# Kernel tuning notes

Hardware: AMD Instinct MI355X
Metric: run time of the kernel (lower is better)

The kernel has to match this reference:

```python
import jax, jax.numpy as jnp
import numpy as np

L = 4          # n_layers
D_MODEL = 512
D_STATE = 32
D_INNER = 1024  # expand=2
D_CONV = 4
DT_RANK = 32    # ceil(d_model/16)
B = 8
T = 512


def setup_inputs() -> dict:
    key = jax.random.key(0)
    ks = jax.random.split(key, 12)
    s = 0.02
    x = jax.random.normal(ks[0], (B, T, D_MODEL), jnp.float32)
    in_w = jax.random.normal(ks[1], (L, D_MODEL, 2 * D_INNER), jnp.float32) * s
    conv_w = jax.random.normal(ks[2], (L, D_INNER, D_CONV), jnp.float32) * s
    conv_b = jnp.zeros((L, D_INNER), jnp.float32)
    xproj_w = jax.random.normal(ks[3], (L, D_INNER, DT_RANK + 2 * D_STATE), jnp.float32) * s
    dt_w = jax.random.normal(ks[4], (L, DT_RANK, D_INNER), jnp.float32) * s
    dt_b = jax.random.normal(ks[5], (L, D_INNER), jnp.float32) * 0.1
    # S4D-real init: A_log = log(1..d_state) per channel
    A_log = jnp.log(jnp.broadcast_to(jnp.arange(1, D_STATE + 1, dtype=jnp.float32), (L, D_INNER, D_STATE)))
    Dp = jnp.ones((L, D_INNER), jnp.float32)
    layer_out_w = jax.random.normal(ks[6], (L, D_INNER, D_MODEL), jnp.float32) * s
    ln_w = jnp.ones((L, D_MODEL), jnp.float32)
    ln_b = jnp.zeros((L, D_MODEL), jnp.float32)
    proj_w = jax.random.normal(ks[7], (D_MODEL, D_MODEL), jnp.float32) * s
    proj_b = jnp.zeros((D_MODEL,), jnp.float32)
    return dict(x=x, in_w=in_w, conv_w=conv_w, conv_b=conv_b, xproj_w=xproj_w,
                dt_w=dt_w, dt_b=dt_b, A_log=A_log, Dp=Dp, layer_out_w=layer_out_w,
                ln_w=ln_w, ln_b=ln_b, proj_w=proj_w, proj_b=proj_b)


def _layernorm(x, w, b, eps=1e-5):
    mu = jnp.mean(x, axis=-1, keepdims=True)
    var = jnp.mean(jnp.square(x - mu), axis=-1, keepdims=True)
    return (x - mu) * jax.lax.rsqrt(var + eps) * w + b


def _selective_scan(u, delta, A, Bm, Cm, D):
    # u, delta: (B,T,di); A: (di,ds); Bm, Cm: (B,T,ds); D: (di,)
    def step(h, inp):
        d_t, B_t, C_t, u_t = inp                      # (B,di),(B,ds),(B,ds),(B,di)
        dA = jnp.exp(d_t[..., None] * A)               # (B,di,ds)
        h = dA * h + (d_t * u_t)[..., None] * B_t[:, None, :]
        y = jnp.einsum('bdn,bn->bd', h, C_t)
        return h, y
    h0 = jnp.zeros((u.shape[0], A.shape[0], A.shape[1]), u.dtype)
    xs = (jnp.swapaxes(delta, 0, 1), jnp.swapaxes(Bm, 0, 1),
          jnp.swapaxes(Cm, 0, 1), jnp.swapaxes(u, 0, 1))
    _, ys = jax.lax.scan(step, h0, xs)                 # ys: (T,B,di)
    return jnp.swapaxes(ys, 0, 1) + u * D


def _mamba_layer(x, in_w, conv_w, conv_b, xproj_w, dt_w, dt_b, A_log, D, out_w):
    xz = x @ in_w                                      # (B,T,2*di)
    u, z = jnp.split(xz, 2, axis=-1)
    # causal depthwise conv1d over time
    uc = jnp.swapaxes(u, 1, 2)                         # (B,di,T)
    uc = jnp.pad(uc, ((0, 0), (0, 0), (D_CONV - 1, 0)))
    uc = jax.lax.conv_general_dilated(
        uc, conv_w[:, None, :], (1,), 'VALID',
        feature_group_count=D_INNER,
        dimension_numbers=('NCH', 'OIH', 'NCH')) + conv_b[None, :, None]
    u = jax.nn.silu(jnp.swapaxes(uc, 1, 2))            # (B,T,di)
    x_dbl = u @ xproj_w                                # (B,T,dt_rank+2*ds)
    dt, Bm, Cm = jnp.split(x_dbl, [DT_RANK, DT_RANK + D_STATE], axis=-1)
    delta = jax.nn.softplus(dt @ dt_w + dt_b)          # (B,T,di)
    A = -jnp.exp(A_log)                                # (di,ds)
    y = _selective_scan(u, delta, A, Bm, Cm, D)
    y = y * jax.nn.silu(z)
    return y @ out_w                                   # (B,T,d_model)


def reference(x, in_w, conv_w, conv_b, xproj_w, dt_w, dt_b, A_log, Dp,
              layer_out_w, ln_w, ln_b, proj_w, proj_b):
    for i in range(L):
        h = _layernorm(x, ln_w[i], ln_b[i])
        x = _mamba_layer(h, in_w[i], conv_w[i], conv_b[i], xproj_w[i],
                         dt_w[i], dt_b[i], A_log[i], Dp[i], layer_out_w[i]) + x
    return x @ proj_w + proj_b
```

## Files before the change

### kernel.cpp

```cpp
#include <hip/hip_runtime.h>
#include <math.h>

#define LNUM 4
#define DM 512
#define DS 32
#define DI 1024
#define DTR 32
#define NB 8
#define NT 512
#define MROWS (NB*NT)
#define NCH (NB*DI)
#define NCK 32
#define TCH (NT/NCK)
#define SSTR 257
#define L2E 1.44269504f

typedef __attribute__((ext_vector_type(8))) short short8;
typedef __attribute__((ext_vector_type(4))) float floatx4;
typedef unsigned short ushort_t;

__device__ __forceinline__ float sigmoidf_(float x){ return 1.f/(1.f+__expf(-x)); }
__device__ __forceinline__ float exp2f_(float x){ return __builtin_amdgcn_exp2f(x); }
__device__ __forceinline__ float bf2f(ushort_t u){ return __uint_as_float(((unsigned)u)<<16); }

__device__ __forceinline__ unsigned short rne_bf16(float f){
  unsigned int u = __float_as_uint(f);
  u += 0x7fffu + ((u >> 16) & 1u);
  return (unsigned short)(u >> 16);
}

__device__ __forceinline__ void load_lds16(const void* g, void* l){
  __builtin_amdgcn_global_load_lds(
      (const __attribute__((address_space(1))) void*)g,
      (__attribute__((address_space(3))) void*)l, 16, 0, 0);
}

__global__ __launch_bounds__(256) void lnz_k(const float* __restrict__ x,
    const float* __restrict__ w, const float* __restrict__ b,
    ushort_t* __restrict__ out, float* __restrict__ xdbl)
{
  int bid = blockIdx.x;
  if (bid >= MROWS){
    int g = (bid - MROWS)*256 + threadIdx.x;
    ((floatx4*)xdbl)[g] = (floatx4){0.f,0.f,0.f,0.f};
    return;
  }
  const float* xr = x + (size_t)bid*DM;
  float v0 = xr[threadIdx.x];
  float v1 = xr[threadIdx.x + 256];
  float s = v0+v1, sq = v0*v0+v1*v1;
  #pragma unroll
  for (int off=32; off>0; off>>=1) { s += __shfl_xor(s, off, 64); sq += __shfl_xor(sq, off, 64); }
  __shared__ float ls[4], lq[4];
  int wid = threadIdx.x >> 6;
  if ((threadIdx.x & 63)==0){ ls[wid]=s; lq[wid]=sq; }
  __syncthreads();
  s  = ls[0]+ls[1]+ls[2]+ls[3];
  sq = lq[0]+lq[1]+lq[2]+lq[3];
  float mean = s * (1.f/DM);
  float var  = sq * (1.f/DM) - mean*mean;
  float rstd = rsqrtf(var + 1e-5f);
  int c0 = threadIdx.x, c1 = threadIdx.x+256;
  out[(size_t)bid*DM + c0] = rne_bf16((v0-mean)*rstd*w[c0] + b[c0]);
  out[(size_t)bid*DM + c1] = rne_bf16((v1-mean)*rstd*w[c1] + b[c1]);
}

__global__ __launch_bounds__(256) void wprep_k(const float* __restrict__ src,
    ushort_t* __restrict__ dst, int K, int N)
{
  src += (size_t)blockIdx.z * K * N;
  dst += (size_t)blockIdx.z * N * K;
  int n0 = blockIdx.x * 64, k0 = blockIdx.y * 64;
  __shared__ float t[64][65];
  int tid = threadIdx.x;
  int cr = tid >> 6, cc = tid & 63;
  #pragma unroll
  for (int i=0;i<16;i++){
    int k = k0 + i*4 + cr, n = n0 + cc;
    float v = (k < K && n < N) ? src[(size_t)k*N + n] : 0.f;
    t[i*4+cr][cc] = v;
  }
  __syncthreads();
  #pragma unroll
  for (int i=0;i<16;i++){
    int n = n0 + i*4 + cr, k = k0 + cc;
    if (n < N && k < K) dst[(size_t)n*K + k] = rne_bf16(t[cc][i*4+cr]);
  }
}

__global__ __launch_bounds__(256) void tbf_k(const ushort_t* __restrict__ src,
    ushort_t* __restrict__ dst)
{
  __shared__ ushort_t tile[64][72];
  int m0 = blockIdx.x * 64;
  int d0 = blockIdx.y * 64;
  int tid = threadIdx.x;
  int lr = tid >> 2;
  int lc = (tid & 3) * 16;
  #pragma unroll
  for (int j=0;j<2;j++){
    short8 v = *(const short8*)&src[(size_t)(m0+lr)*DI + d0 + lc + j*8];
    *(short8*)&tile[lr][lc + j*8] = v;
  }
  __syncthreads();
  int b  = m0 >> 9;
  int t0 = m0 & (NT-1);
  int dgl = tid >> 5;
  int ml  = tid & 31;
  size_t grow = ((size_t)b*128 + (d0>>3) + dgl) * (NT*8);
  #pragma unroll
  for (int i=0;i<2;i++){
    int mm = ml + i*32;
    short8 v = *(const short8*)&tile[mm][dgl*8];
    *(short8*)&dst[grow + (size_t)(t0+mm)*8] = v;
  }
}

enum { AE_SPLIT=0, AE_STORE=1, AE_RESIDBF=2, AE_BIAS=3 };

template<int BN, int FN, int EPI>
__global__ __launch_bounds__(256) void agemm_k(
    const ushort_t* __restrict__ A, int K,
    const ushort_t* __restrict__ Wt,
    float* __restrict__ C0, ushort_t* __restrict__ Zb,
    ushort_t* __restrict__ Cb, int ldc,
    const float* __restrict__ bias)
{
  constexpr int WN = BN/2;
  constexpr int LW4 = BN/32;
  __shared__ __align__(16) ushort_t As[128*64];
  __shared__ __align__(16) ushort_t Ws[BN*64];
  int tid = threadIdx.x;
  int w = tid >> 6, lane = tid & 63;
  int wr = w >> 1, wc = w & 1;
  int quad = lane >> 4, l16 = lane & 15;
  int mBase = blockIdx.y * 128;
  int nBase = blockIdx.x * BN;

  int lr = lane >> 3, ls = lane & 7;
  int sg = ls ^ lr;

  const ushort_t* gA[4]; ushort_t* lA[4];
  #pragma unroll
  for (int j=0;j<4;j++){
    int r0 = (w*4+j)*8;
    gA[j] = A + (size_t)(mBase + r0 + lr)*K + sg*8;
    lA[j] = &As[r0*64];
  }
  const ushort_t* gW[LW4]; ushort_t* lW[LW4];
  #pragma unroll
  for (int c=0;c<LW4;c++){
    int r0 = (w*LW4+c)*8;
    gW[c] = Wt + (size_t)(nBase + r0 + lr)*K + sg*8;
    lW[c] = &Ws[r0*64];
  }

  floatx4 acc[4][FN];
  #pragma unroll
  for (int i=0;i<4;i++)
    #pragma unroll
    for (int j=0;j<FN;j++) acc[i][j] = (floatx4){0.f,0.f,0.f,0.f};

  for (int it=0; it<K; it+=64){
    #pragma unroll
    for (int j=0;j<4;j++) load_lds16(gA[j], lA[j]);
    #pragma unroll
    for (int c=0;c<LW4;c++) load_lds16(gW[c], lW[c]);
    __syncthreads();
    #pragma unroll
    for (int ks=0;ks<2;ks++){
      short8 aF[4], bF[FN];
      #pragma unroll
      for (int i=0;i<4;i++)
        aF[i] = *(const short8*)&As[(wr*64+i*16+l16)*64 + ((((ks<<2)|quad))^(l16&7))*8];
      #pragma unroll
      for (int j=0;j<FN;j++)
        bF[j] = *(const short8*)&Ws[(wc*WN+j*16+l16)*64 + ((((ks<<2)|quad))^(l16&7))*8];
      #pragma unroll
      for (int i=0;i<4;i++)
        #pragma unroll
        for (int j=0;j<FN;j++)
          acc[i][j] = __builtin_amdgcn_mfma_f32_16x16x32_bf16(aF[i], bF[j], acc[i][j], 0, 0, 0);
    }
    __syncthreads();
    #pragma unroll
    for (int j=0;j<4;j++) gA[j] += 64;
    #pragma unroll
    for (int c=0;c<LW4;c++) gW[c] += 64;
  }

  #pragma unroll
  for (int i=0;i<4;i++){
    #pragma unroll
    for (int j=0;j<FN;j++){
      int n = nBase + wc*WN + j*16 + l16;
      int m0i = mBase + wr*64 + i*16 + quad*4;
      if (EPI == AE_SPLIT){
        if (n < DI){
          #pragma unroll
          for (int r=0;r<4;r++) C0[(size_t)(m0i+r)*DI + n] = acc[i][j][r];
        } else {
          int bb = m0i >> 9, tt0 = m0i & (NT-1);
          int nz = n - DI;
          size_t zbase = ((size_t)bb*128 + (nz>>3))*(NT*8) + (nz&7);
          #pragma unroll
          for (int r=0;r<4;r++)
            Zb[zbase + (size_t)(tt0+r)*8] = rne_bf16(acc[i][j][r]);
        }
      } else {
        #pragma unroll
        for (int r=0;r<4;r++){
          int m = m0i + r;
          float v = acc[i][j][r];
          if (EPI == AE_STORE)       { C0[(size_t)m*ldc + n] = v; }
          else if (EPI == AE_RESIDBF){ float nv = C0[(size_t)m*ldc + n] + v;
                                       C0[(size_t)m*ldc + n] = nv;
                                       Cb[(size_t)m*ldc + n] = rne_bf16(nv); }
          else                       { C0[(size_t)m*ldc + n] = v + bias[n]; }
        }
      }
    }
  }
}

__global__ __launch_bounds__(256) void agemm_splitk_k(
    const ushort_t* __restrict__ A, int K, int kseg,
    const ushort_t* __restrict__ Wt, float* __restrict__ C0, int ldc)
{
  constexpr int BN = 96, FN = 3, WN = 48, LW4 = 3;
  __shared__ __align__(16) ushort_t As[128*64];
  __shared__ __align__(16) ushort_t Ws[BN*64];
  int tid = threadIdx.x;
  int w = tid >> 6, lane = tid & 63;
  int wr = w >> 1, wc = w & 1;
  int quad = lane >> 4, l16 = lane & 15;
  int mBase = blockIdx.y * 128;
  int kOff = blockIdx.z * kseg;

  int lr = lane >> 3, ls = lane & 7;
  int sg = ls ^ lr;

  const ushort_t* gA[4]; ushort_t* lA[4];
  #pragma unroll
  for (int j=0;j<4;j++){
    int r0 = (w*4+j)*8;
    gA[j] = A + (size_t)(mBase + r0 + lr)*K + kOff + sg*8;
    lA[j] = &As[r0*64];
  }
  const ushort_t* gW[LW4]; ushort_t* lW[LW4];
  #pragma unroll
  for (int c=0;c<LW4;c++){
    int r0 = (w*LW4+c)*8;
    gW[c] = Wt + (size_t)(r0 + lr)*K + kOff + sg*8;
    lW[c] = &Ws[r0*64];
  }
  floatx4 acc[4][FN];
  #pragma unroll
  for (int i=0;i<4;i++)
    #pragma unroll
    for (int j=0;j<FN;j++) acc[i][j] = (floatx4){0.f,0.f,0.f,0.f};

  for (int it=0; it<kseg; it+=64){
    #pragma unroll
    for (int j=0;j<4;j++) load_lds16(gA[j], lA[j]);
    #pragma unroll
    for (int c=0;c<LW4;c++) load_lds16(gW[c], lW[c]);
    __syncthreads();
    #pragma unroll
    for (int ks=0;ks<2;ks++){
      short8 aF[4], bF[FN];
      #pragma unroll
      for (int i=0;i<4;i++)
        aF[i] = *(const short8*)&As[(wr*64+i*16+l16)*64 + ((((ks<<2)|quad))^(l16&7))*8];
      #pragma unroll
      for (int j=0;j<FN;j++)
        bF[j] = *(const short8*)&Ws[(wc*WN+j*16+l16)*64 + ((((ks<<2)|quad))^(l16&7))*8];
      #pragma unroll
      for (int i=0;i<4;i++)
        #pragma unroll
        for (int j=0;j<FN;j++)
          acc[i][j] = __builtin_amdgcn_mfma_f32_16x16x32_bf16(aF[i], bF[j], acc[i][j], 0, 0, 0);
    }
    __syncthreads();
    #pragma unroll
    for (int j=0;j<4;j++) gA[j] += 64;
    #pragma unroll
    for (int c=0;c<LW4;c++) gW[c] += 64;
  }
  #pragma unroll
  for (int i=0;i<4;i++){
    #pragma unroll
    for (int j=0;j<FN;j++){
      int n = wc*WN + j*16 + l16;
      #pragma unroll
      for (int r=0;r<4;r++){
        int m = mBase + wr*64 + i*16 + quad*4 + r;
        atomicAdd(&C0[(size_t)m*ldc + n], acc[i][j][r]);
      }
    }
  }
}

__global__ __launch_bounds__(256) void gemm32_k(
    const float* __restrict__ A, int lda, int K,
    const ushort_t* __restrict__ Wt,
    float* __restrict__ C0, int ldc, const float* __restrict__ bias)
{
  constexpr int STR = 40;
  __shared__ __align__(16) short As[128*STR];
  __shared__ __align__(16) short Ws[128*STR];
  int tid = threadIdx.x;
  int w = tid >> 6, lane = tid & 63;
  int wr = w >> 1, wc = w & 1;
  int quad = lane >> 4, l16 = lane & 15;
  int mBase = blockIdx.y * 128;
  int nBase = blockIdx.x * 128;

  floatx4 acc[4][4];
  #pragma unroll
  for (int i=0;i<4;i++)
    #pragma unroll
    for (int j=0;j<4;j++) acc[i][j] = (floatx4){0.f,0.f,0.f,0.f};

  int sRow = tid >> 3, kv = tid & 7;
  for (int k0 = 0; k0 < K; k0 += 32) {
    #pragma unroll
    for (int i=0;i<4;i++){
      int r = sRow + i*32;
      floatx4 v = *(const floatx4*)&A[(size_t)(mBase+r)*lda + k0 + kv*4];
      unsigned int p0 = (unsigned int)rne_bf16(v.x) | ((unsigned int)rne_bf16(v.y) << 16);
      unsigned int p1 = (unsigned int)rne_bf16(v.z) | ((unsigned int)rne_bf16(v.w) << 16);
      uint2 pk; pk.x = p0; pk.y = p1;
      *(uint2*)&As[r*STR + kv*4] = pk;
    }
    #pragma unroll
    for (int i=0;i<4;i++){
      int r = sRow + i*32;
      uint2 wv = *(const uint2*)&Wt[(size_t)(nBase+r)*K + k0 + kv*4];
      *(uint2*)&Ws[r*STR + kv*4] = wv;
    }
    __syncthreads();
    short8 aF[4], bF[4];
    #pragma unroll
    for (int i=0;i<4;i++)
      aF[i] = *(const short8*)&As[(wr*64 + i*16 + l16)*STR + quad*8];
    #pragma unroll
    for (int j=0;j<4;j++)
      bF[j] = *(const short8*)&Ws[(wc*64 + j*16 + l16)*STR + quad*8];
    #pragma unroll
    for (int i=0;i<4;i++)
      #pragma unroll
      for (int j=0;j<4;j++)
        acc[i][j] = __builtin_amdgcn_mfma_f32_16x16x32_bf16(aF[i], bF[j], acc[i][j], 0, 0, 0);
    __syncthreads();
  }
  #pragma unroll
  for (int i=0;i<4;i++){
    #pragma unroll
    for (int j=0;j<4;j++){
      int n = nBase + wc*64 + j*16 + l16;
      int m0i = mBase + wr*64 + i*16 + quad*4;
      int bb = m0i >> 9, tt0 = m0i & (NT-1);
      size_t gbase = ((size_t)bb*128 + (n>>3))*(NT*8) + (n&7);
      #pragma unroll
      for (int r=0;r<4;r++){
        float t = acc[i][j][r] + bias[n];
        float sp = (t > 20.f) ? t : log1pf(__expf(t));
        C0[gbase + (size_t)(tt0+r)*8] = sp;
      }
    }
  }
}

__global__ __launch_bounds__(256) void conv_k(const float* __restrict__ u,
    const float* __restrict__ cw, const float* __restrict__ cb,
    ushort_t* __restrict__ ucbf)
{
  int g = blockIdx.x*256 + threadIdx.x;
  int d = g & (DI-1);
  int m = g >> 10;
  int t = m & (NT-1);
  float w0=cw[d*4+0], w1=cw[d*4+1], w2=cw[d*4+2], w3=cw[d*4+3];
  float acc = cb[d];
  acc += w3 * u[(size_t)m*DI + d];
  if (t>=1) acc += w2*u[(size_t)(m-1)*DI+d];
  if (t>=2) acc += w1*u[(size_t)(m-2)*DI+d];
  if (t>=3) acc += w0*u[(size_t)(m-3)*DI+d];
  float s = acc * sigmoidf_(acc);
  ucbf[(size_t)m*DI+d] = rne_bf16(s);
}

__global__ __launch_bounds__(256,2) void scan_fused_k(
    const float* __restrict__ dl_t, const ushort_t* __restrict__ uc_t,
    const ushort_t* __restrict__ zb_t, const float* __restrict__ xdbl,
    const float* __restrict__ Dp, ushort_t* __restrict__ y)
{
  __shared__ float Hl[DS*SSTR];
  __shared__ float Sl[256];
  int tid = threadIdx.x;
  int ci = tid & 7, ck = tid >> 3;
  int dg = blockIdx.x & 127;
  int b  = blockIdx.x >> 7;
  int d  = dg*8 + ci;
  int tbase = ck*TCH;
  size_t grp = ((size_t)b*128 + dg)*(NT*8);

  const float*   dp = dl_t + grp + tbase*8 + ci;
  const ushort_t* up = uc_t + grp + tbase*8 + ci;
  const ushort_t* zp = zb_t + grp + tbase*8 + ci;
  const float*   xb = xdbl + ((size_t)b*NT + tbase)*96;

  float h[DS];
  #pragma unroll
  for (int n=0;n<DS;n++) h[n]=0.f;
  float S = 0.f;
  #pragma unroll 4
  for (int t=0;t<TCH;t++){
    float dv = dp[t*8];
    float uv = bf2f(up[t*8]);
    floatx4 Bv[8];
    const floatx4* Br = (const floatx4*)(xb + (size_t)t*96 + 32);
    #pragma unroll
    for (int j=0;j<8;j++) Bv[j] = Br[j];
    float q = exp2f_(dv * -L2E);
    float du = dv*uv;
    S += dv;
    float q2=q*q, q4=q2*q2, q8=q4*q4, q16=q8*q8;
    float eg[4];
    eg[0]=q; eg[1]=q8*q; eg[2]=q16*q; eg[3]=q16*eg[1];
    #pragma unroll
    for (int j=0;j<4;j++){
      #pragma unroll
      for (int n=0;n<8;n++){
        int s = j*8+n;
        float Bs = ((const float*)&Bv[s>>2])[s&3];
        h[s] = fmaf(eg[j], h[s], du*Bs);
        eg[j] *= q;
      }
    }
  }
  Sl[tid] = S;
  #pragma unroll
  for (int n=0;n<DS;n++) Hl[n*SSTR + tid] = h[n];
  __syncthreads();

  {
    int s   = tid & 31;
    int ci2 = tid >> 5;
    float hp = 0.f;
    float coef = -(float)(s+1)*L2E;
    #pragma unroll
    for (int c=0;c<NCK;c++){
      float Sc = Sl[c*8 + ci2];
      float Hc = Hl[s*SSTR + c*8 + ci2];
      float E  = exp2f_(coef*Sc);
      Hl[s*SSTR + c*8 + ci2] = hp;
      hp = fmaf(E, hp, Hc);
    }
  }
  __syncthreads();

  #pragma unroll
  for (int n=0;n<DS;n++) h[n] = Hl[n*SSTR + tid];
  float Dv = Dp[d];
  ushort_t* yp = y + ((size_t)(b*NT + tbase))*DI + d;
  #pragma unroll 4
  for (int t=0;t<TCH;t++){
    float dv = dp[t*8];
    float uv = bf2f(up[t*8]);
    float zv = bf2f(zp[t*8]);
    floatx4 Bv[8], Cv[8];
    const floatx4* Br = (const floatx4*)(xb + (size_t)t*96 + 32);
    const floatx4* Cr = (const floatx4*)(xb + (size_t)t*96 + 64);
    #pragma unroll
    for (int j=0;j<8;j++){ Bv[j]=Br[j]; Cv[j]=Cr[j]; }
    float q = exp2f_(dv * -L2E);
    float du = dv*uv;
    float q2=q*q, q4=q2*q2, q8=q4*q4, q16=q8*q8;
    float eg[4];
    eg[0]=q; eg[1]=q8*q; eg[2]=q16*q; eg[3]=q16*eg[1];
    float pacc[4] = {0.f,0.f,0.f,0.f};
    #pragma unroll
    for (int j=0;j<4;j++){
      #pragma unroll
      for (int n=0;n<8;n++){
        int s = j*8+n;
        float Bs = ((const float*)&Bv[s>>2])[s&3];
        float Cs = ((const float*)&Cv[s>>2])[s&3];
        h[s] = fmaf(eg[j], h[s], du*Bs);
        pacc[j] = fmaf(h[s], Cs, pacc[j]);
        eg[j] *= q;
      }
    }
    float acc = (pacc[0]+pacc[1]) + (pacc[2]+pacc[3]);
    float yv = acc + uv*Dv;
    yp[(size_t)t*DI] = rne_bf16(yv * (zv * sigmoidf_(zv)));
  }
}

extern "C" void kernel_launch(void* const* d_in, const int* in_sizes, int n_in,
                              void* d_out, int out_size, void* d_ws, size_t ws_size,
                              hipStream_t stream) {
  const float* x       = (const float*)d_in[0];
  const float* in_w    = (const float*)d_in[1];
  const float* conv_w  = (const float*)d_in[2];
  const float* conv_b  = (const float*)d_in[3];
  const float* xproj_w = (const float*)d_in[4];
  const float* dt_w    = (const float*)d_in[5];
  const float* dt_b    = (const float*)d_in[6];
  const float* Dp      = (const float*)d_in[8];
  const float* low     = (const float*)d_in[9];
  const float* ln_w    = (const float*)d_in[10];
  const float* ln_b    = (const float*)d_in[11];
  const float* proj_w  = (const float*)d_in[12];
  const float* proj_b  = (const float*)d_in[13];
  float* out = (float*)d_out;

  float* ws   = (float*)d_ws;
  float* xcur = ws;
  float* u0   = xcur + (size_t)MROWS*DM;
  float* xdbl = u0   + (size_t)MROWS*DI;
  float* dl   = xdbl + (size_t)MROWS*96;
  ushort_t* hn_bf   = (ushort_t*)(dl + (size_t)MROWS*DI);
  ushort_t* zb_bf   = hn_bf   + (size_t)MROWS*DM;
  ushort_t* ucb_bf  = zb_bf   + (size_t)MROWS*DI;
  ushort_t* xcur_bf = ucb_bf  + (size_t)MROWS*DI;
  ushort_t* inw_t   = xcur_bf + (size_t)MROWS*DM;
  ushort_t* xprj_t  = inw_t  + (size_t)LNUM*2*DI*DM;
  ushort_t* dtw_t   = xprj_t + (size_t)LNUM*96*DI;
  ushort_t* low_t   = dtw_t  + (size_t)LNUM*DI*DTR;
  ushort_t* prj_t   = low_t  + (size_t)LNUM*DM*DI;
  ushort_t* uct_bf  = prj_t  + (size_t)DM*DM;
  ushort_t* y_bf = (ushort_t*)u0;

  hipMemcpyAsync(xcur, x, sizeof(float)*(size_t)MROWS*DM, hipMemcpyDeviceToDevice, stream);

  wprep_k<<<dim3(32, 8, LNUM), 256, 0, stream>>>(in_w,    inw_t,  DM, 2*DI);
  wprep_k<<<dim3(2, 16, LNUM), 256, 0, stream>>>(xproj_w, xprj_t, DI, 96);
  wprep_k<<<dim3(16, 1, LNUM), 256, 0, stream>>>(dt_w,    dtw_t,  DTR, DI);
  wprep_k<<<dim3(8, 16, LNUM), 256, 0, stream>>>(low,     low_t,  DI, DM);
  wprep_k<<<dim3(8, 8, 1),     256, 0, stream>>>(proj_w,  prj_t,  DM, DM);

  for (int l=0; l<LNUM; l++){
    lnz_k<<<MROWS + (MROWS*96/4)/256, 256, 0, stream>>>(
        xcur, ln_w + l*DM, ln_b + l*DM, hn_bf, xdbl);
    agemm_k<128,4,AE_SPLIT><<<dim3(16,32), 256, 0, stream>>>(
        hn_bf, DM, inw_t + (size_t)l*2*DI*DM, u0, zb_bf, nullptr, 0, nullptr);
    conv_k<<<(MROWS*DI)/256, 256, 0, stream>>>(u0, conv_w + l*DI*4, conv_b + l*DI, ucb_bf);
    tbf_k<<<dim3(MROWS/64, DI/64), 256, 0, stream>>>(ucb_bf, uct_bf);
    agemm_splitk_k<<<dim3(1,32,4), 256, 0, stream>>>(
        ucb_bf, DI, DI/4, xprj_t + (size_t)l*96*DI, xdbl, 96);
    gemm32_k<<<dim3(8,32), 256, 0, stream>>>(
        xdbl, 96, DTR, dtw_t + (size_t)l*DI*DTR, dl, DI, dt_b + l*DI);
    scan_fused_k<<<NCH/8, 256, 0, stream>>>(
        dl, uct_bf, zb_bf, xdbl, Dp + l*DI, y_bf);
    agemm_k<128,4,AE_RESIDBF><<<dim3(4,32), 256, 0, stream>>>(
        y_bf, DI, low_t + (size_t)l*DM*DI, xcur, nullptr, xcur_bf, DM, nullptr);
  }
  agemm_k<128,4,AE_BIAS><<<dim3(4,32), 256, 0, stream>>>(
      xcur_bf, DM, prj_t, out, nullptr, nullptr, DM, proj_b);
}
```

Baseline: 849.4 us.

## Replace LDS chunk-carry scan with warp-shuffle scan; fuse transpose into conv

The cross-chunk state carry in the selective scan moves from a serial 32-step LDS pass, run by a different thread mapping, to a wavefront shuffle-based parallel prefix combine. Only the last chunk of each wavefront goes through a small LDS buffer, and a short serial loop over up to three wavefronts finishes the carry. This cuts the large LDS footprint and one barrier, which may raise occupancy, but adds exp and shuffle work in each prefix step. Separately, the conv kernel now writes the transposed bf16 layout itself, so the tbf_k transpose launch goes away at the cost of scattered 2-byte stores.

```diff
diff --git a/kernel.cpp b/kernel.cpp
--- a/kernel.cpp
+++ b/kernel.cpp
@@ -12,7 +12,6 @@
 #define NCH (NB*DI)
 #define NCK 32
 #define TCH (NT/NCK)
-#define SSTR 257
 #define L2E 1.44269504f
 
 typedef __attribute__((ext_vector_type(8))) short short8;
@@ -85,34 +84,6 @@
   for (int i=0;i<16;i++){
     int n = n0 + i*4 + cr, k = k0 + cc;
     if (n < N && k < K) dst[(size_t)n*K + k] = rne_bf16(t[cc][i*4+cr]);
-  }
-}
-
-__global__ __launch_bounds__(256) void tbf_k(const ushort_t* __restrict__ src,
-    ushort_t* __restrict__ dst)
-{
-  __shared__ ushort_t tile[64][72];
-  int m0 = blockIdx.x * 64;
-  int d0 = blockIdx.y * 64;
-  int tid = threadIdx.x;
-  int lr = tid >> 2;
-  int lc = (tid & 3) * 16;
-  #pragma unroll
-  for (int j=0;j<2;j++){
-    short8 v = *(const short8*)&src[(size_t)(m0+lr)*DI + d0 + lc + j*8];
-    *(short8*)&tile[lr][lc + j*8] = v;
-  }
-  __syncthreads();
-  int b  = m0 >> 9;
-  int t0 = m0 & (NT-1);
-  int dgl = tid >> 5;
-  int ml  = tid & 31;
-  size_t grow = ((size_t)b*128 + (d0>>3) + dgl) * (NT*8);
-  #pragma unroll
-  for (int i=0;i<2;i++){
-    int mm = ml + i*32;
-    short8 v = *(const short8*)&tile[mm][dgl*8];
-    *(short8*)&dst[grow + (size_t)(t0+mm)*8] = v;
   }
 }
 
@@ -374,7 +345,7 @@
 
 __global__ __launch_bounds__(256) void conv_k(const float* __restrict__ u,
     const float* __restrict__ cw, const float* __restrict__ cb,
-    ushort_t* __restrict__ ucbf)
+    ushort_t* __restrict__ ucbf, ushort_t* __restrict__ uct)
 {
   int g = blockIdx.x*256 + threadIdx.x;
   int d = g & (DI-1);
@@ -387,7 +358,9 @@
   if (t>=2) acc += w1*u[(size_t)(m-2)*DI+d];
   if (t>=3) acc += w0*u[(size_t)(m-3)*DI+d];
   float s = acc * sigmoidf_(acc);
-  ucbf[(size_t)m*DI+d] = rne_bf16(s);
+  ushort_t sv = rne_bf16(s);
+  ucbf[(size_t)m*DI+d] = sv;
+  uct[((size_t)(m>>9)*128 + (d>>3))*(NT*8) + (size_t)t*8 + (d&7)] = sv;
 }
 
 __global__ __launch_bounds__(256,2) void scan_fused_k(
@@ -395,9 +368,11 @@
     const ushort_t* __restrict__ zb_t, const float* __restrict__ xdbl,
     const float* __restrict__ Dp, ushort_t* __restrict__ y)
 {
-  __shared__ float Hl[DS*SSTR];
-  __shared__ float Sl[256];
+  __shared__ float LW[4*DS*8];
+  __shared__ float LS[4*8];
   int tid = threadIdx.x;
+  int lane = tid & 63;
+  int wv = tid >> 6;
   int ci = tid & 7, ck = tid >> 3;
   int dg = blockIdx.x & 127;
   int b  = blockIdx.x >> 7;
@@ -427,7 +402,7 @@
     S += dv;
     float q2=q*q, q4=q2*q2, q8=q4*q4, q16=q8*q8;
     float eg[4];
-    eg[0]=q; eg[1]=q8*q; eg[2]=q16*q; eg[3]=q16*eg[1];
+    eg[0]=q; eg[1]=q8*q; eg[2]=q16*q; eg[3]=q16*q8*q;
     #pragma unroll
     for (int j=0;j<4;j++){
       #pragma unroll
@@ -439,29 +414,65 @@
       }
     }
   }
-  Sl[tid] = S;
-  #pragma unroll
-  for (int n=0;n<DS;n++) Hl[n*SSTR + tid] = h[n];
+
+  #pragma unroll
+  for (int off=8; off<64; off<<=1){
+    float Sp = __shfl_up(S, off);
+    bool ok = (lane >= off);
+    float q = exp2f_(S * -L2E);
+    float q2=q*q, q4=q2*q2, q8=q4*q4, q16=q8*q8;
+    float eg[4];
+    eg[0]=q; eg[1]=q8*q; eg[2]=q16*q; eg[3]=q16*q8*q;
+    if (!ok){ eg[0]=0.f; eg[1]=0.f; eg[2]=0.f; eg[3]=0.f; }
+    #pragma unroll
+    for (int j=0;j<4;j++){
+      #pragma unroll
+      for (int n=0;n<8;n++){
+        int s = j*8+n;
+        float hp = __shfl_up(h[s], off);
+        h[s] = fmaf(eg[j], hp, h[s]);
+        eg[j] *= q;
+      }
+    }
+    if (ok) S += Sp;
+  }
+
+  if ((lane >> 3) == 7){
+    #pragma unroll
+    for (int n=0;n<DS;n++) LW[(wv*DS + n)*8 + ci] = h[n];
+    LS[wv*8 + ci] = S;
+  }
+  {
+    float Sp = __shfl_up(S, 8);
+    bool ok = (lane >= 8);
+    #pragma unroll
+    for (int n=0;n<DS;n++){
+      float hp = __shfl_up(h[n], 8);
+      h[n] = ok ? hp : 0.f;
+    }
+    S = ok ? Sp : 0.f;
+  }
   __syncthreads();
-
   {
-    int s   = tid & 31;
-    int ci2 = tid >> 5;
-    float hp = 0.f;
-    float coef = -(float)(s+1)*L2E;
-    #pragma unroll
-    for (int c=0;c<NCK;c++){
-      float Sc = Sl[c*8 + ci2];
-      float Hc = Hl[s*SSTR + c*8 + ci2];
-      float E  = exp2f_(coef*Sc);
-      Hl[s*SSTR + c*8 + ci2] = hp;
-      hp = fmaf(E, hp, Hc);
-    }
-  }
-  __syncthreads();
-
-  #pragma unroll
-  for (int n=0;n<DS;n++) h[n] = Hl[n*SSTR + tid];
+    float Sacc = S;
+    for (int wp = wv-1; wp >= 0; --wp){
+      float q = exp2f_(Sacc * -L2E);
+      float q2=q*q, q4=q2*q2, q8=q4*q4, q16=q8*q8;
+      float eg[4];
+      eg[0]=q; eg[1]=q8*q; eg[2]=q16*q; eg[3]=q16*q8*q;
+      #pragma unroll
+      for (int j=0;j<4;j++){
+        #pragma unroll
+        for (int n=0;n<8;n++){
+          int s = j*8+n;
+          h[s] = fmaf(eg[j], LW[(wp*DS + s)*8 + ci], h[s]);
+          eg[j] *= q;
+        }
+      }
+      Sacc += LS[wp*8 + ci];
+    }
+  }
+
   float Dv = Dp[d];
   ushort_t* yp = y + ((size_t)(b*NT + tbase))*DI + d;
   #pragma unroll 4
@@ -478,7 +489,7 @@
     float du = dv*uv;
     float q2=q*q, q4=q2*q2, q8=q4*q4, q16=q8*q8;
     float eg[4];
-    eg[0]=q; eg[1]=q8*q; eg[2]=q16*q; eg[3]=q16*eg[1];
+    eg[0]=q; eg[1]=q8*q; eg[2]=q16*q; eg[3]=q16*q8*q;
     float pacc[4] = {0.f,0.f,0.f,0.f};
     #pragma unroll
     for (int j=0;j<4;j++){
@@ -546,8 +557,7 @@
         xcur, ln_w + l*DM, ln_b + l*DM, hn_bf, xdbl);
     agemm_k<128,4,AE_SPLIT><<<dim3(16,32), 256, 0, stream>>>(
         hn_bf, DM, inw_t + (size_t)l*2*DI*DM, u0, zb_bf, nullptr, 0, nullptr);
-    conv_k<<<(MROWS*DI)/256, 256, 0, stream>>>(u0, conv_w + l*DI*4, conv_b + l*DI, ucb_bf);
-    tbf_k<<<dim3(MROWS/64, DI/64), 256, 0, stream>>>(ucb_bf, uct_bf);
+    conv_k<<<(MROWS*DI)/256, 256, 0, stream>>>(u0, conv_w + l*DI*4, conv_b + l*DI, ucb_bf, uct_bf);
     agemm_splitk_k<<<dim3(1,32,4), 256, 0, stream>>>(
         ucb_bf, DI, DI/4, xprj_t + (size_t)l*96*DI, xdbl, 96);
     gemm32_k<<<dim3(8,32), 256, 0, stream>>>(
```

Measured after the change: 843.2 us. No clear change (-0.7%).
